# Kernel optimization log

Measured on AMD Instinct MI355X. Metric: run time of the kernel, lower is better.

The kernel has to match this reference:

```python
import jax, jax.numpy as jnp
import numpy as np

D_MODEL = 1024
N_HEAD = 16
HEAD_DIM = D_MODEL // N_HEAD
BATCH = 2
SEQ = 2048


def setup_inputs() -> dict:
    key = jax.random.key(0)
    ks = jax.random.split(key, 5)
    std = np.sqrt(2.0 / (D_MODEL + D_MODEL)).astype(np.float32)
    return {
        "in_features": jax.random.normal(ks[0], (BATCH, SEQ, D_MODEL), dtype=jnp.float32),
        "Wq": jax.random.normal(ks[1], (D_MODEL, D_MODEL), dtype=jnp.float32) * std,
        "Wk": jax.random.normal(ks[2], (D_MODEL, D_MODEL), dtype=jnp.float32) * std,
        "Wv": jax.random.normal(ks[3], (D_MODEL, D_MODEL), dtype=jnp.float32) * std,
        "Wo": jax.random.normal(ks[4], (D_MODEL, D_MODEL), dtype=jnp.float32) * std,
    }


def reference(in_features, Wq, Wk, Wv, Wo):
    B, S, _ = in_features.shape
    # projections: x @ W (custom Linear stores weight as [in, out], no bias)
    q = (in_features @ Wq).reshape(B, S, N_HEAD, HEAD_DIM).transpose(0, 2, 1, 3)  # [B,H,S,Dh]
    k = (in_features @ Wk).reshape(B, S, N_HEAD, HEAD_DIM).transpose(0, 2, 1, 3)
    v = (in_features @ Wv).reshape(B, S, N_HEAD, HEAD_DIM).transpose(0, 2, 1, 3)
    scale = HEAD_DIM ** (-0.5)
    scores = jnp.einsum("bhqd,bhkd->bhqk", q, k) * scale  # [B,H,S,S]
    causal = jnp.tril(jnp.ones((S, S), dtype=bool))
    scores = jnp.where(causal, scores, -jnp.inf)
    attn = jax.nn.softmax(scores, axis=-1)
    ctx = jnp.einsum("bhqk,bhkd->bhqd", attn, v)  # [B,H,S,Dh]
    ctx = ctx.transpose(0, 2, 1, 3).reshape(B, S, D_MODEL)
    return ctx @ Wo
```

## Files before the change

kernel.cpp:

```cpp
#include <hip/hip_runtime.h>
#include <hip/hip_bf16.h>

#define DM 1024
#define NH 16
#define HD 64
#define B_ 2
#define S_ 2048
#define M_ (B_*S_)

typedef __attribute__((ext_vector_type(8))) short bf16x8;
typedef __attribute__((ext_vector_type(4))) float f32x4;

__device__ __forceinline__ float bf2f(ushort u) {
  union { unsigned u32; float f; } c; c.u32 = ((unsigned)u) << 16; return c.f;
}
__device__ __forceinline__ ushort f2bf(float f) {
  union { float f; unsigned u32; } c; c.f = f;
  unsigned u = c.u32;
  unsigned r = (u + 0x7fffu + ((u >> 16) & 1u)) >> 16;
  return (ushort)r;
}
__device__ __forceinline__ unsigned fbits(float f) {
  union { float f; unsigned u; } c; c.f = f; return c.u;
}

__device__ __forceinline__ void async16(const ushort* g, ushort* l) {
  __builtin_amdgcn_global_load_lds((const __attribute__((address_space(1))) void*)g,
                                   (__attribute__((address_space(3))) void*)l, 16, 0, 0);
}

__global__ void cvt_prep(const float* __restrict__ x, const float* __restrict__ W0,
                         const float* __restrict__ W1, const float* __restrict__ W2,
                         const float* __restrict__ W3, ushort* __restrict__ wt,
                         ushort* __restrict__ xb) {
  __shared__ float tile[64][65];
  int z = blockIdx.z;
  int tx = threadIdx.x, ty = threadIdx.y;
  if (z == 4) {
    int tid = ty * 64 + tx;
    size_t base4 = ((size_t)blockIdx.y * 16 + blockIdx.x) * 4096;
    const float4* xv = (const float4*)x;
    ushort4* ov = (ushort4*)xb;
    #pragma unroll
    for (int k = 0; k < 16; ++k) {
      float4 v = xv[base4 + k * 256 + tid];
      ushort4 o;
      o.x = f2bf(v.x); o.y = f2bf(v.y); o.z = f2bf(v.z); o.w = f2bf(v.w);
      ov[base4 + k * 256 + tid] = o;
    }
    return;
  }
  const float* W = (z == 0) ? W0 : (z == 1) ? W1 : (z == 2) ? W2 : W3;
  ushort* Wt = wt + (size_t)z * (DM * DM);
  int c0 = blockIdx.x * 64, r0 = blockIdx.y * 64;
  #pragma unroll
  for (int i = ty; i < 64; i += 4) tile[i][tx] = W[(size_t)(r0 + i) * DM + c0 + tx];
  __syncthreads();
  #pragma unroll
  for (int i = ty; i < 64; i += 4) Wt[(size_t)(c0 + i) * DM + r0 + tx] = f2bf(tile[tx][i]);
}

template <int MODE, int BN>
__device__ __forceinline__ void gemm_body(const ushort* __restrict__ A,
                                          const ushort* __restrict__ Bt,
                                          ushort* __restrict__ Cb,
                                          float* __restrict__ Cf,
                                          ushort* As, ushort* Bs, ushort* Ts) {
  const int K = DM;
  constexpr int CN = BN / 32;
  int m0 = blockIdx.y * 128;
  int n0 = blockIdx.x * BN;
  int t = threadIdx.x;
  int lane = t & 63, wave = t >> 6;
  int wm = (wave >> 1) * 64, wn = (wave & 1) * (BN / 2);
  int lrow = lane & 15, quad = lane >> 4;

  int Ra = wave * 32;
  int Rb = wave * (BN / 4);
  int srow = lane >> 2, scol = (lane & 3) * 8;

  f32x4 acc[4][CN];
  #pragma unroll
  for (int r = 0; r < 4; ++r)
    #pragma unroll
    for (int c = 0; c < CN; ++c) acc[r][c] = (f32x4){0.f, 0.f, 0.f, 0.f};

  for (int k0 = 0; k0 < K; k0 += 32) {
    const ushort* ga = A + (size_t)(m0 + Ra + srow) * K + k0 + scol;
    const ushort* gb = Bt + (size_t)(n0 + Rb + srow) * K + k0 + scol;
    async16(ga,          As + Ra * 32);
    async16(ga + 16 * K, As + (Ra + 16) * 32);
    async16(gb,          Bs + Rb * 32);
    if (BN == 128) async16(gb + 16 * K, Bs + (Rb + 16) * 32);
    __syncthreads();

    bf16x8 af[4], bfr[CN];
    #pragma unroll
    for (int r = 0; r < 4; ++r)
      af[r] = *(const bf16x8*)(As + (wm + r * 16 + lrow) * 32 + quad * 8);
    #pragma unroll
    for (int c = 0; c < CN; ++c)
      bfr[c] = *(const bf16x8*)(Bs + (wn + c * 16 + lrow) * 32 + quad * 8);
    #pragma unroll
    for (int r = 0; r < 4; ++r)
      #pragma unroll
      for (int c = 0; c < CN; ++c)
        acc[r][c] = __builtin_amdgcn_mfma_f32_16x16x32_bf16(af[r], bfr[c], acc[r][c], 0, 0, 0);
    __syncthreads();
  }

  if constexpr (MODE == 2) {
    int bb = m0 >> 11;
    int s0base = m0 & 2047;
    #pragma unroll
    for (int H = 0; H < 2; ++H) {
      __syncthreads();
      if ((wave >> 1) == H) {
        #pragma unroll
        for (int r = 0; r < 4; ++r)
          #pragma unroll
          for (int c = 0; c < 4; ++c) {
            uint2 pk;
            pk.x = (unsigned)f2bf(acc[r][c][0]) | ((unsigned)f2bf(acc[r][c][1]) << 16);
            pk.y = (unsigned)f2bf(acc[r][c][2]) | ((unsigned)f2bf(acc[r][c][3]) << 16);
            *(uint2*)(Ts + (wn + c * 16 + lrow) * 72 + r * 16 + quad * 4) = pk;
          }
      }
      __syncthreads();
      #pragma unroll
      for (int i = 0; i < 4; ++i) {
        int id = t + i * 256;
        int nn = id >> 3, col = (id & 7) * 8;
        uint4 v = *(const uint4*)(Ts + nn * 72 + col);
        int h2 = (n0 >> 6) + (nn >> 6), d2 = nn & 63;
        size_t dst = (((size_t)(bb * NH + h2)) * HD + d2) * (size_t)S_ + s0base + H * 64 + col;
        *(uint4*)(Cb + dst) = v;
      }
    }
  } else {
    #pragma unroll
    for (int r = 0; r < 4; ++r) {
      #pragma unroll
      for (int c = 0; c < CN; ++c) {
        #pragma unroll
        for (int e = 0; e < 4; ++e) {
          int m = m0 + wm + r * 16 + quad * 4 + e;
          int n = n0 + wn + c * 16 + lrow;
          if (MODE == 0) {
            Cf[(size_t)m * DM + n] = acc[r][c][e];
          } else {
            int b = m >> 11, s = m & 2047, h = n >> 6, d = n & 63;
            Cb[(((size_t)(b * NH + h)) * S_ + s) * HD + d] = f2bf(acc[r][c][e]);
          }
        }
      }
    }
  }
}

__global__ __launch_bounds__(256, 2) void gemm_qkv(const ushort* __restrict__ A,
                                                   const ushort* __restrict__ wt,
                                                   ushort* __restrict__ qkv) {
  __shared__ __align__(16) ushort smem[9216];
  ushort* As = smem;
  ushort* Bs = smem + 4096;
  ushort* Ts = smem;
  int z = blockIdx.z;
  if (z < 2)
    gemm_body<1, 128>(A, wt + (size_t)z * (DM * DM), qkv + (size_t)z * ((size_t)M_ * DM),
                      nullptr, As, Bs, Ts);
  else
    gemm_body<2, 128>(A, wt + (size_t)2 * (DM * DM), qkv + (size_t)2 * ((size_t)M_ * DM),
                      nullptr, As, Bs, Ts);
}

__global__ __launch_bounds__(256, 2) void gemm_out(const ushort* __restrict__ A,
                                                   const ushort* __restrict__ wt,
                                                   float* __restrict__ C) {
  __shared__ __align__(16) ushort As[128 * 32];
  __shared__ __align__(16) ushort Bs[64 * 32];
  gemm_body<0, 64>(A, wt, nullptr, C, As, Bs, nullptr);
}

#define EXPC 0.18033688011f

struct AttnState {
  f32x4 o[4];
  float l;
};

template <bool MASKED>
__device__ __forceinline__ void attn_tile_compute(
    int q0, int kt, bf16x8 qf0, bf16x8 qf1,
    const bf16x8 kf0[4], const bf16x8 kf1[4],
    const bf16x8 vf0[4], const bf16x8 vf1[4],
    ushort* pl, AttnState& st, int lrow, int quad) {
  f32x4 s[4];
  #pragma unroll
  for (int c = 0; c < 4; ++c) {
    f32x4 z = (f32x4){0.f, 0.f, 0.f, 0.f};
    z = __builtin_amdgcn_mfma_f32_16x16x32_bf16(kf0[c], qf0, z, 0, 0, 0);
    z = __builtin_amdgcn_mfma_f32_16x16x32_bf16(kf1[c], qf1, z, 0, 0, 0);
    s[c] = z;
  }
  int q = q0 + lrow;
  #pragma unroll
  for (int c = 0; c < 4; ++c) {
    float pv[4];
    #pragma unroll
    for (int e = 0; e < 4; ++e) {
      float v = __builtin_amdgcn_exp2f(s[c][e] * EXPC);
      if (MASKED) {
        int key = kt + c * 16 + quad * 4 + e;
        v = (key <= q) ? v : 0.f;
      }
      pv[e] = v;
      st.l += v;
    }
    uint2 pk;
    pk.x = __builtin_amdgcn_perm(fbits(pv[1]), fbits(pv[0]), 0x07060302u);
    pk.y = __builtin_amdgcn_perm(fbits(pv[3]), fbits(pv[2]), 0x07060302u);
    *(uint2*)(pl + lrow * 72 + c * 16 + quad * 4) = pk;
  }
  bf16x8 pf0 = *(const bf16x8*)(pl + lrow * 72 + quad * 8);
  bf16x8 pf1 = *(const bf16x8*)(pl + lrow * 72 + 32 + quad * 8);
  #pragma unroll
  for (int dt = 0; dt < 4; ++dt) {
    st.o[dt] = __builtin_amdgcn_mfma_f32_16x16x32_bf16(pf0, vf0[dt], st.o[dt], 0, 0, 0);
    st.o[dt] = __builtin_amdgcn_mfma_f32_16x16x32_bf16(pf1, vf1[dt], st.o[dt], 0, 0, 0);
  }
}

__global__ __launch_bounds__(256, 2) void attn_mfma(const ushort* __restrict__ Q,
                                                    const ushort* __restrict__ Kmat,
                                                    const ushort* __restrict__ Vt,
                                                    ushort* __restrict__ ctx) {
  __shared__ __align__(16) ushort Ks[2][64 * 72];
  __shared__ __align__(16) ushort Vs[2][64 * 72];
  __shared__ __align__(16) ushort plds[8][16 * 72];
  int t = threadIdx.x;
  int lane = t & 63, wave = t >> 6;
  int lrow = lane & 15, quad = lane >> 4;
  int bh = blockIdx.y;
  int p = blockIdx.x;
  int qt_lo = p, qt_hi = 31 - p;
  const ushort* Kb = Kmat + (size_t)bh * S_ * HD;
  const ushort* Vb = Vt + (size_t)bh * HD * S_;
  ushort* pl_hi = plds[wave];
  ushort* pl_lo = plds[wave + 4];
  int b = bh >> 4, h = bh & 15;

  int r0 = t >> 3, s0 = (t & 7) * 8;
  int r1 = (t + 256) >> 3, s1 = s0;

  int q0_lo = qt_lo * 64 + wave * 16;
  int q0_hi = qt_hi * 64 + wave * 16;
  const ushort* Qlo = Q + ((size_t)bh * S_ + q0_lo) * HD;
  const ushort* Qhi = Q + ((size_t)bh * S_ + q0_hi) * HD;
  bf16x8 qlo0 = *(const bf16x8*)(Qlo + (size_t)lrow * HD + quad * 8);
  bf16x8 qlo1 = *(const bf16x8*)(Qlo + (size_t)lrow * HD + 32 + quad * 8);
  bf16x8 qhi0 = *(const bf16x8*)(Qhi + (size_t)lrow * HD + quad * 8);
  bf16x8 qhi1 = *(const bf16x8*)(Qhi + (size_t)lrow * HD + 32 + quad * 8);

  AttnState lo, hi;
  #pragma unroll
  for (int i = 0; i < 4; ++i) {
    lo.o[i] = (f32x4){0.f, 0.f, 0.f, 0.f}; hi.o[i] = (f32x4){0.f, 0.f, 0.f, 0.f};
  }
  lo.l = 0.f; hi.l = 0.f;

  int kend = qt_hi * 64;
  int lo_end = qt_lo * 64;

  {
    uint4 ka = *(const uint4*)(Kb + (size_t)r0 * HD + s0);
    uint4 kb2 = *(const uint4*)(Kb + (size_t)r1 * HD + s1);
    uint4 va = *(const uint4*)(Vb + (size_t)r0 * S_ + s0);
    uint4 vb2 = *(const uint4*)(Vb + (size_t)r1 * S_ + s1);
    *(uint4*)(Ks[0] + r0 * 72 + s0) = ka;
    *(uint4*)(Ks[0] + r1 * 72 + s1) = kb2;
    *(uint4*)(Vs[0] + r0 * 72 + s0) = va;
    *(uint4*)(Vs[0] + r1 * 72 + s1) = vb2;
  }
  __syncthreads();

  for (int kt = 0; kt <= kend; kt += 64) {
    int cur = (kt >> 6) & 1, nxt = cur ^ 1;
    bool has_next = (kt < kend);

    uint4 ka, kb2, va, vb2;
    if (has_next) {
      int ktn = kt + 64;
      ka  = *(const uint4*)(Kb + (size_t)(ktn + r0) * HD + s0);
      kb2 = *(const uint4*)(Kb + (size_t)(ktn + r1) * HD + s1);
      va  = *(const uint4*)(Vb + (size_t)r0 * S_ + ktn + s0);
      vb2 = *(const uint4*)(Vb + (size_t)r1 * S_ + ktn + s1);
    }

    bf16x8 kf0[4], kf1[4], vf0[4], vf1[4];
    #pragma unroll
    for (int c = 0; c < 4; ++c) {
      const ushort* kr = Ks[cur] + (c * 16 + lrow) * 72;
      kf0[c] = *(const bf16x8*)(kr + quad * 8);
      kf1[c] = *(const bf16x8*)(kr + 32 + quad * 8);
      const ushort* vr = Vs[cur] + (c * 16 + lrow) * 72;
      vf0[c] = *(const bf16x8*)(vr + quad * 8);
      vf1[c] = *(const bf16x8*)(vr + 32 + quad * 8);
    }

    if (kt < kend)
      attn_tile_compute<false>(q0_hi, kt, qhi0, qhi1, kf0, kf1, vf0, vf1, pl_hi, hi, lrow, quad);
    else
      attn_tile_compute<true>(q0_hi, kt, qhi0, qhi1, kf0, kf1, vf0, vf1, pl_hi, hi, lrow, quad);
    if (kt < lo_end)
      attn_tile_compute<false>(q0_lo, kt, qlo0, qlo1, kf0, kf1, vf0, vf1, pl_lo, lo, lrow, quad);
    else if (kt == lo_end)
      attn_tile_compute<true>(q0_lo, kt, qlo0, qlo1, kf0, kf1, vf0, vf1, pl_lo, lo, lrow, quad);

    if (has_next) {
      *(uint4*)(Ks[nxt] + r0 * 72 + s0) = ka;
      *(uint4*)(Ks[nxt] + r1 * 72 + s1) = kb2;
      *(uint4*)(Vs[nxt] + r0 * 72 + s0) = va;
      *(uint4*)(Vs[nxt] + r1 * 72 + s1) = vb2;
    }
    __syncthreads();
  }

  #pragma unroll
  for (int half = 0; half < 2; ++half) {
    AttnState& st = half ? hi : lo;
    int q0 = half ? q0_hi : q0_lo;
    float l = st.l;
    l += __shfl_xor(l, 16);
    l += __shfl_xor(l, 32);
    float rl = 1.0f / l;
    #pragma unroll
    for (int e = 0; e < 4; ++e) {
      float rinv = __shfl(rl, quad * 4 + e);
      int q = q0 + quad * 4 + e;
      #pragma unroll
      for (int dt = 0; dt < 4; ++dt)
        ctx[((size_t)b * S_ + q) * DM + h * HD + dt * 16 + lrow] = f2bf(st.o[dt][e] * rinv);
    }
  }
}

extern "C" void kernel_launch(void* const* d_in, const int* in_sizes, int n_in,
                              void* d_out, int out_size, void* d_ws, size_t ws_size,
                              hipStream_t stream) {
  const float* x  = (const float*)d_in[0];
  const float* Wq = (const float*)d_in[1];
  const float* Wk = (const float*)d_in[2];
  const float* Wv = (const float*)d_in[3];
  const float* Wo = (const float*)d_in[4];
  float* out = (float*)d_out;
  ushort* ws = (ushort*)d_ws;

  ushort* xb  = ws;
  ushort* wt  = xb + (size_t)M_ * DM;
  ushort* qkv = wt + (size_t)4 * DM * DM;
  ushort* ctx = qkv + (size_t)3 * M_ * DM;

  cvt_prep<<<dim3(16, 16, 5), dim3(64, 4), 0, stream>>>(x, Wq, Wk, Wv, Wo, wt, xb);
  gemm_qkv<<<dim3(DM / 128, M_ / 128, 3), 256, 0, stream>>>(xb, wt, qkv);
  attn_mfma<<<dim3(16, B_ * NH), 256, 0, stream>>>(qkv, qkv + (size_t)M_ * DM,
                                                   qkv + (size_t)2 * M_ * DM, ctx);
  gemm_out<<<dim3(DM / 64, M_ / 128), 256, 0, stream>>>(ctx, wt + (size_t)3 * DM * DM, out);
}
```

Before: 183.2 us.

## Switch attention to 32x32x16 MFMA with XOR-swizzled LDS and two-wave blocks

The attention kernel now uses 32x32x16 bf16 MFMA instead of 16x16x32. Each wave handles 32 query rows, and a block has 2 waves (128 threads) instead of 4. Padded LDS rows of stride 72 are replaced by an XOR swizzle on stride-64 rows for K, V and P, and K/V fragments are read from LDS inside the compute routine rather than preloaded. This aims to cut the number of MFMA issues and LDS traffic per FLOP, but it halves threads per block with launch_bounds(128,1), which lowers latency hiding and raises register pressure.

```diff
diff --git a/kernel.cpp b/kernel.cpp
--- a/kernel.cpp
+++ b/kernel.cpp
@@ -10,6 +10,7 @@
 
 typedef __attribute__((ext_vector_type(8))) short bf16x8;
 typedef __attribute__((ext_vector_type(4))) float f32x4;
+typedef __attribute__((ext_vector_type(16))) float f32x16;
 
 __device__ __forceinline__ float bf2f(ushort u) {
   union { unsigned u32; float f; } c; c.u32 = ((unsigned)u) << 16; return c.f;
@@ -185,102 +186,109 @@
 #define EXPC 0.18033688011f
 
 struct AttnState {
-  f32x4 o[4];
+  f32x16 o[2];
   float l;
 };
 
 template <bool MASKED>
-__device__ __forceinline__ void attn_tile_compute(
-    int q0, int kt, bf16x8 qf0, bf16x8 qf1,
-    const bf16x8 kf0[4], const bf16x8 kf1[4],
-    const bf16x8 vf0[4], const bf16x8 vf1[4],
-    ushort* pl, AttnState& st, int lrow, int quad) {
-  f32x4 s[4];
-  #pragma unroll
-  for (int c = 0; c < 4; ++c) {
-    f32x4 z = (f32x4){0.f, 0.f, 0.f, 0.f};
-    z = __builtin_amdgcn_mfma_f32_16x16x32_bf16(kf0[c], qf0, z, 0, 0, 0);
-    z = __builtin_amdgcn_mfma_f32_16x16x32_bf16(kf1[c], qf1, z, 0, 0, 0);
+__device__ __forceinline__ void attn_tile_compute32(
+    int q0, int kt, const bf16x8 qf[4],
+    const ushort* Kc, const ushort* Vc, ushort* pl,
+    AttnState& st, int m31, int hi) {
+  f32x16 s[2];
+  #pragma unroll
+  for (int c = 0; c < 2; ++c) {
+    f32x16 z = {0.f};
+    #pragma unroll
+    for (int f = 0; f < 4; ++f) {
+      int row = c * 32 + m31;
+      bf16x8 kf = *(const bf16x8*)(Kc + row * 64 + (((2 * f + hi) ^ (row & 7)) * 8));
+      z = __builtin_amdgcn_mfma_f32_32x32x16_bf16(kf, qf[f], z, 0, 0, 0);
+    }
     s[c] = z;
   }
-  int q = q0 + lrow;
-  #pragma unroll
-  for (int c = 0; c < 4; ++c) {
-    float pv[4];
-    #pragma unroll
-    for (int e = 0; e < 4; ++e) {
-      float v = __builtin_amdgcn_exp2f(s[c][e] * EXPC);
-      if (MASKED) {
-        int key = kt + c * 16 + quad * 4 + e;
-        v = (key <= q) ? v : 0.f;
-      }
-      pv[e] = v;
-      st.l += v;
-    }
-    uint2 pk;
-    pk.x = __builtin_amdgcn_perm(fbits(pv[1]), fbits(pv[0]), 0x07060302u);
-    pk.y = __builtin_amdgcn_perm(fbits(pv[3]), fbits(pv[2]), 0x07060302u);
-    *(uint2*)(pl + lrow * 72 + c * 16 + quad * 4) = pk;
-  }
-  bf16x8 pf0 = *(const bf16x8*)(pl + lrow * 72 + quad * 8);
-  bf16x8 pf1 = *(const bf16x8*)(pl + lrow * 72 + 32 + quad * 8);
-  #pragma unroll
-  for (int dt = 0; dt < 4; ++dt) {
-    st.o[dt] = __builtin_amdgcn_mfma_f32_16x16x32_bf16(pf0, vf0[dt], st.o[dt], 0, 0, 0);
-    st.o[dt] = __builtin_amdgcn_mfma_f32_16x16x32_bf16(pf1, vf1[dt], st.o[dt], 0, 0, 0);
-  }
-}
-
-__global__ __launch_bounds__(256, 2) void attn_mfma(const ushort* __restrict__ Q,
+  int q = q0 + m31;
+  #pragma unroll
+  for (int c = 0; c < 2; ++c) {
+    #pragma unroll
+    for (int g = 0; g < 4; ++g) {
+      int kbase = kt + c * 32 + g * 8 + hi * 4;
+      float pv[4];
+      #pragma unroll
+      for (int e = 0; e < 4; ++e) {
+        float v = __builtin_amdgcn_exp2f(s[c][g * 4 + e] * EXPC);
+        if (MASKED) v = (kbase + e <= q) ? v : 0.f;
+        pv[e] = v;
+        st.l += v;
+      }
+      uint2 pk;
+      pk.x = __builtin_amdgcn_perm(fbits(pv[1]), fbits(pv[0]), 0x07060302u);
+      pk.y = __builtin_amdgcn_perm(fbits(pv[3]), fbits(pv[2]), 0x07060302u);
+      *(uint2*)(pl + m31 * 64 + (((g + 4 * c) ^ (m31 & 7)) * 8) + hi * 4) = pk;
+    }
+  }
+  bf16x8 pf[4];
+  #pragma unroll
+  for (int f = 0; f < 4; ++f)
+    pf[f] = *(const bf16x8*)(pl + m31 * 64 + (((2 * f + hi) ^ (m31 & 7)) * 8));
+  #pragma unroll
+  for (int db = 0; db < 2; ++db) {
+    f32x16 z = st.o[db];
+    #pragma unroll
+    for (int f = 0; f < 4; ++f) {
+      int rv = db * 32 + m31;
+      bf16x8 vf = *(const bf16x8*)(Vc + rv * 64 + (((2 * f + hi) ^ (rv & 7)) * 8));
+      z = __builtin_amdgcn_mfma_f32_32x32x16_bf16(pf[f], vf, z, 0, 0, 0);
+    }
+    st.o[db] = z;
+  }
+}
+
+__global__ __launch_bounds__(128, 1) void attn_mfma(const ushort* __restrict__ Q,
                                                     const ushort* __restrict__ Kmat,
                                                     const ushort* __restrict__ Vt,
                                                     ushort* __restrict__ ctx) {
-  __shared__ __align__(16) ushort Ks[2][64 * 72];
-  __shared__ __align__(16) ushort Vs[2][64 * 72];
-  __shared__ __align__(16) ushort plds[8][16 * 72];
+  __shared__ __align__(16) ushort Ks[2][64 * 64];
+  __shared__ __align__(16) ushort Vs[2][64 * 64];
+  __shared__ __align__(16) ushort plds[4][32 * 64];
   int t = threadIdx.x;
   int lane = t & 63, wave = t >> 6;
-  int lrow = lane & 15, quad = lane >> 4;
+  int m31 = lane & 31, hi = lane >> 5;
   int bh = blockIdx.y;
   int p = blockIdx.x;
   int qt_lo = p, qt_hi = 31 - p;
   const ushort* Kb = Kmat + (size_t)bh * S_ * HD;
   const ushort* Vb = Vt + (size_t)bh * HD * S_;
-  ushort* pl_hi = plds[wave];
-  ushort* pl_lo = plds[wave + 4];
+  ushort* pl_hi = plds[wave * 2];
+  ushort* pl_lo = plds[wave * 2 + 1];
   int b = bh >> 4, h = bh & 15;
 
-  int r0 = t >> 3, s0 = (t & 7) * 8;
-  int r1 = (t + 256) >> 3, s1 = s0;
-
-  int q0_lo = qt_lo * 64 + wave * 16;
-  int q0_hi = qt_hi * 64 + wave * 16;
-  const ushort* Qlo = Q + ((size_t)bh * S_ + q0_lo) * HD;
-  const ushort* Qhi = Q + ((size_t)bh * S_ + q0_hi) * HD;
-  bf16x8 qlo0 = *(const bf16x8*)(Qlo + (size_t)lrow * HD + quad * 8);
-  bf16x8 qlo1 = *(const bf16x8*)(Qlo + (size_t)lrow * HD + 32 + quad * 8);
-  bf16x8 qhi0 = *(const bf16x8*)(Qhi + (size_t)lrow * HD + quad * 8);
-  bf16x8 qhi1 = *(const bf16x8*)(Qhi + (size_t)lrow * HD + 32 + quad * 8);
-
-  AttnState lo, hi;
-  #pragma unroll
-  for (int i = 0; i < 4; ++i) {
-    lo.o[i] = (f32x4){0.f, 0.f, 0.f, 0.f}; hi.o[i] = (f32x4){0.f, 0.f, 0.f, 0.f};
-  }
-  lo.l = 0.f; hi.l = 0.f;
+  int c8t = t & 7;
+  int rbase = t >> 3;
+
+  int q0_lo = qt_lo * 64 + wave * 32;
+  int q0_hi = qt_hi * 64 + wave * 32;
+  bf16x8 qlo[4], qhi[4];
+  #pragma unroll
+  for (int f = 0; f < 4; ++f) {
+    qlo[f] = *(const bf16x8*)(Q + ((size_t)bh * S_ + q0_lo + m31) * HD + f * 16 + hi * 8);
+    qhi[f] = *(const bf16x8*)(Q + ((size_t)bh * S_ + q0_hi + m31) * HD + f * 16 + hi * 8);
+  }
+
+  AttnState lo, hi_s;
+  #pragma unroll
+  for (int i = 0; i < 2; ++i) { lo.o[i] = (f32x16){0.f}; hi_s.o[i] = (f32x16){0.f}; }
+  lo.l = 0.f; hi_s.l = 0.f;
 
   int kend = qt_hi * 64;
   int lo_end = qt_lo * 64;
 
-  {
-    uint4 ka = *(const uint4*)(Kb + (size_t)r0 * HD + s0);
-    uint4 kb2 = *(const uint4*)(Kb + (size_t)r1 * HD + s1);
-    uint4 va = *(const uint4*)(Vb + (size_t)r0 * S_ + s0);
-    uint4 vb2 = *(const uint4*)(Vb + (size_t)r1 * S_ + s1);
-    *(uint4*)(Ks[0] + r0 * 72 + s0) = ka;
-    *(uint4*)(Ks[0] + r1 * 72 + s1) = kb2;
-    *(uint4*)(Vs[0] + r0 * 72 + s0) = va;
-    *(uint4*)(Vs[0] + r1 * 72 + s1) = vb2;
+  #pragma unroll
+  for (int i = 0; i < 4; ++i) {
+    int r = rbase + 16 * i;
+    int so = r * 64 + ((c8t ^ (r & 7)) * 8);
+    *(uint4*)(Ks[0] + so) = *(const uint4*)(Kb + (size_t)r * HD + c8t * 8);
+    *(uint4*)(Vs[0] + so) = *(const uint4*)(Vb + (size_t)r * S_ + c8t * 8);
   }
   __syncthreads();
 
@@ -288,59 +296,54 @@
     int cur = (kt >> 6) & 1, nxt = cur ^ 1;
     bool has_next = (kt < kend);
 
-    uint4 ka, kb2, va, vb2;
+    uint4 kr[4], vr[4];
     if (has_next) {
       int ktn = kt + 64;
-      ka  = *(const uint4*)(Kb + (size_t)(ktn + r0) * HD + s0);
-      kb2 = *(const uint4*)(Kb + (size_t)(ktn + r1) * HD + s1);
-      va  = *(const uint4*)(Vb + (size_t)r0 * S_ + ktn + s0);
-      vb2 = *(const uint4*)(Vb + (size_t)r1 * S_ + ktn + s1);
-    }
-
-    bf16x8 kf0[4], kf1[4], vf0[4], vf1[4];
-    #pragma unroll
-    for (int c = 0; c < 4; ++c) {
-      const ushort* kr = Ks[cur] + (c * 16 + lrow) * 72;
-      kf0[c] = *(const bf16x8*)(kr + quad * 8);
-      kf1[c] = *(const bf16x8*)(kr + 32 + quad * 8);
-      const ushort* vr = Vs[cur] + (c * 16 + lrow) * 72;
-      vf0[c] = *(const bf16x8*)(vr + quad * 8);
-      vf1[c] = *(const bf16x8*)(vr + 32 + quad * 8);
+      #pragma unroll
+      for (int i = 0; i < 4; ++i) {
+        int r = rbase + 16 * i;
+        kr[i] = *(const uint4*)(Kb + (size_t)(ktn + r) * HD + c8t * 8);
+        vr[i] = *(const uint4*)(Vb + (size_t)r * S_ + ktn + c8t * 8);
+      }
     }
 
     if (kt < kend)
-      attn_tile_compute<false>(q0_hi, kt, qhi0, qhi1, kf0, kf1, vf0, vf1, pl_hi, hi, lrow, quad);
+      attn_tile_compute32<false>(q0_hi, kt, qhi, Ks[cur], Vs[cur], pl_hi, hi_s, m31, hi);
     else
-      attn_tile_compute<true>(q0_hi, kt, qhi0, qhi1, kf0, kf1, vf0, vf1, pl_hi, hi, lrow, quad);
+      attn_tile_compute32<true>(q0_hi, kt, qhi, Ks[cur], Vs[cur], pl_hi, hi_s, m31, hi);
     if (kt < lo_end)
-      attn_tile_compute<false>(q0_lo, kt, qlo0, qlo1, kf0, kf1, vf0, vf1, pl_lo, lo, lrow, quad);
+      attn_tile_compute32<false>(q0_lo, kt, qlo, Ks[cur], Vs[cur], pl_lo, lo, m31, hi);
     else if (kt == lo_end)
-      attn_tile_compute<true>(q0_lo, kt, qlo0, qlo1, kf0, kf1, vf0, vf1, pl_lo, lo, lrow, quad);
+      attn_tile_compute32<true>(q0_lo, kt, qlo, Ks[cur], Vs[cur], pl_lo, lo, m31, hi);
 
     if (has_next) {
-      *(uint4*)(Ks[nxt] + r0 * 72 + s0) = ka;
-      *(uint4*)(Ks[nxt] + r1 * 72 + s1) = kb2;
-      *(uint4*)(Vs[nxt] + r0 * 72 + s0) = va;
-      *(uint4*)(Vs[nxt] + r1 * 72 + s1) = vb2;
+      #pragma unroll
+      for (int i = 0; i < 4; ++i) {
+        int r = rbase + 16 * i;
+        int so = r * 64 + ((c8t ^ (r & 7)) * 8);
+        *(uint4*)(Ks[nxt] + so) = kr[i];
+        *(uint4*)(Vs[nxt] + so) = vr[i];
+      }
     }
     __syncthreads();
   }
 
   #pragma unroll
   for (int half = 0; half < 2; ++half) {
-    AttnState& st = half ? hi : lo;
+    AttnState& st = half ? hi_s : lo;
     int q0 = half ? q0_hi : q0_lo;
-    float l = st.l;
-    l += __shfl_xor(l, 16);
-    l += __shfl_xor(l, 32);
+    float l = st.l + __shfl_xor(st.l, 32);
     float rl = 1.0f / l;
     #pragma unroll
-    for (int e = 0; e < 4; ++e) {
-      float rinv = __shfl(rl, quad * 4 + e);
-      int q = q0 + quad * 4 + e;
-      #pragma unroll
-      for (int dt = 0; dt < 4; ++dt)
-        ctx[((size_t)b * S_ + q) * DM + h * HD + dt * 16 + lrow] = f2bf(st.o[dt][e] * rinv);
+    for (int g = 0; g < 4; ++g) {
+      #pragma unroll
+      for (int e = 0; e < 4; ++e) {
+        int qlocal = e + g * 8 + hi * 4;
+        float rinv = __shfl(rl, qlocal);
+        size_t base = ((size_t)b * S_ + q0 + qlocal) * DM + h * HD + m31;
+        ctx[base]      = f2bf(st.o[0][g * 4 + e] * rinv);
+        ctx[base + 32] = f2bf(st.o[1][g * 4 + e] * rinv);
+      }
     }
   }
 }
@@ -363,7 +366,7 @@
 
   cvt_prep<<<dim3(16, 16, 5), dim3(64, 4), 0, stream>>>(x, Wq, Wk, Wv, Wo, wt, xb);
   gemm_qkv<<<dim3(DM / 128, M_ / 128, 3), 256, 0, stream>>>(xb, wt, qkv);
-  attn_mfma<<<dim3(16, B_ * NH), 256, 0, stream>>>(qkv, qkv + (size_t)M_ * DM,
+  attn_mfma<<<dim3(16, B_ * NH), 128, 0, stream>>>(qkv, qkv + (size_t)M_ * DM,
                                                    qkv + (size_t)2 * M_ * DM, ctx);
   gemm_out<<<dim3(DM / 64, M_ / 128), 256, 0, stream>>>(ctx, wt + (size_t)3 * DM * DM, out);
 }
```

Result: slower. 221.2 us (+20.8%).
